# Optimization experiments

Hardware: AMD Instinct MI355X
Metric: run time of the kernel (lower is better)

## Reference

```python
import jax, jax.numpy as jnp
import numpy as np

B, S, D = 4, 2048, 1024
E = 16          # num_experts
K = 2           # num_experts_per_tok
F = 512         # moe_intermediate_size
FS = 2048       # shared_expert_intermediate_size


def setup_inputs() -> dict:
    key = jax.random.key(0)
    ks = jax.random.split(key, 9)
    s = 0.02
    return {
        "hidden_states": jax.random.normal(ks[0], (B, S, D), jnp.float32),
        "router_w": jax.random.normal(ks[1], (E, D), jnp.float32) * s,   # torch Linear-style [out,in]
        "Wg": jax.random.normal(ks[2], (E, D, F), jnp.float32) * s,      # gate_proj per expert
        "Wu": jax.random.normal(ks[3], (E, D, F), jnp.float32) * s,      # up_proj per expert
        "Wd": jax.random.normal(ks[4], (E, F, D), jnp.float32) * s,      # down_proj per expert
        "Sg": jax.random.normal(ks[5], (D, FS), jnp.float32) * s,        # shared expert gate_proj
        "Su": jax.random.normal(ks[6], (D, FS), jnp.float32) * s,        # shared expert up_proj
        "Sd": jax.random.normal(ks[7], (FS, D), jnp.float32) * s,        # shared expert down_proj
        "shared_gate_w": jax.random.normal(ks[8], (D, 1), jnp.float32) * s,
    }


def reference(hidden_states, router_w, Wg, Wu, Wd, Sg, Su, Sd, shared_gate_w):
    b, s, d = hidden_states.shape
    x = hidden_states.reshape(-1, d)                      # [T, D]
    T = x.shape[0]

    # --- router (Qwen3NextTopKRouter): fp32 softmax -> topk -> renorm ---
    logits = jnp.einsum("td,ed->te", x.astype(jnp.float32), router_w.astype(jnp.float32))
    probs = jax.nn.softmax(logits, axis=-1)               # [T, E]
    top_w, top_i = jax.lax.top_k(probs, K)                # [T, K]
    top_w = top_w / jnp.sum(top_w, axis=-1, keepdims=True)  # norm_topk_prob
    top_w = top_w.astype(x.dtype)

    # dense combine weights [T, E]: zero except at selected experts (index_add semantics)
    dense_w = jnp.zeros((T, E), x.dtype).at[jnp.arange(T)[:, None], top_i].add(top_w)

    # --- experts: SwiGLU per expert, scan over the fixed expert axis ---
    def body(acc, params):
        wg, wu, wd, cw = params                            # cw: [T]
        h = jax.nn.silu(x @ wg) * (x @ wu)                 # [T, F]
        return acc + cw[:, None] * (h @ wd), None

    expert_out, _ = jax.lax.scan(body, jnp.zeros_like(x), (Wg, Wu, Wd, dense_w.T))

    # --- shared expert with sigmoid gate ---
    shared = (jax.nn.silu(x @ Sg) * (x @ Su)) @ Sd         # [T, D]
    shared = jax.nn.sigmoid(x @ shared_gate_w) * shared

    out = expert_out + shared
    return out.reshape(b, s, d)
```

## Files before the change

kernel.cpp:

```cpp
#include <hip/hip_runtime.h>

typedef __attribute__((ext_vector_type(8))) short short8;
typedef __attribute__((ext_vector_type(4))) float f32x4;
typedef unsigned short u16;
typedef unsigned int u32;

#define DEVI __device__ __forceinline__

DEVI u16 f2b(float f) {
  u32 u = __float_as_uint(f);
  u32 r = u + 0x7FFFu + ((u >> 16) & 1u);
  return (u16)(r >> 16);
}
DEVI float b2f(u16 h) { return __uint_as_float(((u32)h) << 16); }
DEVI float silu(float g) { return g / (1.f + __expf(-g)); }

constexpr int T_ = 8192, D_ = 1024, E_ = 16, F_ = 512, FS_ = 2048;

constexpr size_t OFF_XB   = 0;
constexpr size_t OFF_WGU  = OFF_XB  + (size_t)T_ * D_ * 2;
constexpr size_t OFF_WDT  = OFF_WGU + (size_t)E_ * 2 * F_ * D_ * 2;
constexpr size_t OFF_SGU  = OFF_WDT + (size_t)E_ * D_ * F_ * 2;
constexpr size_t OFF_SDT  = OFF_SGU + (size_t)2 * FS_ * D_ * 2;
constexpr size_t OFF_HB   = OFF_SDT + (size_t)D_ * FS_ * 2;
constexpr size_t OFF_HS   = OFF_HB  + (size_t)2 * T_ * F_ * 2;
constexpr size_t OFF_PAIR = OFF_HS  + (size_t)T_ * FS_ * 2;
constexpr size_t OFF_PW   = OFF_PAIR + (size_t)2 * T_ * D_ * 2;
constexpr size_t OFF_GATE = OFF_PW  + (size_t)2 * T_ * 4;
constexpr size_t OFF_CNT  = OFF_GATE + (size_t)T_ * 4;
constexpr size_t OFF_TOP2 = OFF_CNT + 64;
constexpr size_t OFF_LIST = OFF_TOP2 + (size_t)T_ * 4;

__global__ void prep_kernel(
    const float4* __restrict__ x4, const float4* __restrict__ rw4,
    const float4* __restrict__ sgw4, int* __restrict__ top2e,
    float* __restrict__ pw, float* __restrict__ gate, ushort4* __restrict__ xb4,
    const float* __restrict__ Wg, const float* __restrict__ Wu, const float* __restrict__ Wd,
    const float* __restrict__ Sg, const float* __restrict__ Su, const float* __restrict__ Sd,
    u16* __restrict__ wgu, u16* __restrict__ wdT,
    u16* __restrict__ sgu, u16* __restrict__ sdT) {
  const int tid = threadIdx.x;
  const int bid = blockIdx.x;
  if (bid >= 7680) {
    const int lane = tid & 63, wid = tid >> 6;
    const int t = (bid - 7680) * 4 + wid;
    const float4* xr = x4 + (size_t)t * (D_ / 4);
    float acc[17];
#pragma unroll
    for (int e = 0; e < 17; ++e) acc[e] = 0.f;
    ushort4 xo[4];
#pragma unroll
    for (int j = 0; j < 4; ++j) {
      const int d4 = j * 64 + lane;
      float4 xv = xr[d4];
      xo[j] = make_ushort4(f2b(xv.x), f2b(xv.y), f2b(xv.z), f2b(xv.w));
#pragma unroll
      for (int e = 0; e < 16; ++e) {
        float4 wv = rw4[e * 256 + d4];
        acc[e] = fmaf(xv.x, wv.x, fmaf(xv.y, wv.y, fmaf(xv.z, wv.z, fmaf(xv.w, wv.w, acc[e]))));
      }
      float4 sv = sgw4[d4];
      acc[16] = fmaf(xv.x, sv.x, fmaf(xv.y, sv.y, fmaf(xv.z, sv.z, fmaf(xv.w, sv.w, acc[16]))));
    }
#pragma unroll
    for (int j = 0; j < 4; ++j)
      xb4[(size_t)t * 256 + j * 64 + lane] = xo[j];
#pragma unroll
    for (int e = 0; e < 17; ++e) {
      float v = acc[e];
#pragma unroll
      for (int off = 32; off; off >>= 1) v += __shfl_xor(v, off);
      acc[e] = v;
    }
    if (lane == 0) {
      int i1 = 0; float l1 = acc[0];
#pragma unroll
      for (int e = 1; e < 16; ++e) if (acc[e] > l1) { l1 = acc[e]; i1 = e; }
      int i2 = (i1 == 0) ? 1 : 0; float l2 = acc[i2];
#pragma unroll
      for (int e = 0; e < 16; ++e) {
        if (e == i1) continue;
        if (acc[e] > l2) { l2 = acc[e]; i2 = e; }
      }
      float w1 = 1.f / (1.f + expf(l2 - l1));
      top2e[t] = i1 | (i2 << 8);
      pw[2 * t] = w1;
      pw[2 * t + 1] = 1.f - w1;
      gate[t] = 1.f / (1.f + expf(-acc[16]));
    }
    return;
  }
  __shared__ float lds[64][65];
  int i = bid;
  const float* in; u16* out; int R, C, mode, rem;
  if (i < 6144) {
    int j = i >> 11; rem = i & 2047;
    int b = rem >> 7; rem &= 127;
    if (j == 0)      { in = Wg + (size_t)b * D_ * F_; out = wgu + (size_t)b * 2 * F_ * D_; R = D_; C = F_;  mode = 0; }
    else if (j == 1) { in = Wu + (size_t)b * D_ * F_; out = wgu + (size_t)b * 2 * F_ * D_; R = D_; C = F_;  mode = 1; }
    else             { in = Wd + (size_t)b * F_ * D_; out = wdT + (size_t)b * D_ * F_;     R = F_; C = D_;  mode = 2; }
  } else {
    int r2 = i - 6144; int j = r2 >> 9; rem = r2 & 511;
    if (j == 0)      { in = Sg; out = sgu; R = D_;  C = FS_; mode = 0; }
    else if (j == 1) { in = Su; out = sgu; R = D_;  C = FS_; mode = 1; }
    else             { in = Sd; out = sdT; R = FS_; C = D_;  mode = 2; }
  }
  const int ntx = C >> 6;
  const int cx = rem % ntx, cy = rem / ntx;
  const int c0 = cx * 64, r0 = cy * 64;
  {
    const int tx4 = (tid & 15) * 4, ty = tid >> 4;
#pragma unroll
    for (int p = 0; p < 4; ++p) {
      const int rr = ty + p * 16;
      float4 v = *(const float4*)&in[(size_t)(r0 + rr) * C + c0 + tx4];
      lds[rr][tx4] = v.x; lds[rr][tx4 + 1] = v.y; lds[rr][tx4 + 2] = v.z; lds[rr][tx4 + 3] = v.w;
    }
  }
  __syncthreads();
  {
    const int ol = tid >> 2, seg = tid & 3;
    const int f = c0 + ol;
    size_t orow;
    if (mode == 2) orow = f;
    else orow = (size_t)((f >> 4) << 5) + (f & 15) + (mode == 1 ? 16 : 0);
    u16 vals[16];
#pragma unroll
    for (int k = 0; k < 16; ++k) vals[k] = f2b(lds[seg * 16 + k][ol]);
    u16* dst = out + orow * R + r0 + seg * 16;
    *(short8*)dst = *(short8*)&vals[0];
    *(short8*)(dst + 8) = *(short8*)&vals[8];
  }
}

__global__ __launch_bounds__(1024) void compact_kernel(
    const int* __restrict__ top2e, int* __restrict__ lists, int* __restrict__ counts) {
  const int e = blockIdx.x;
  const int tid = threadIdx.x, lane = tid & 63, wid = tid >> 6;
  __shared__ int wsum[16];
  __shared__ int base;
  if (tid == 0) base = 0;
  __syncthreads();
  for (int c0 = 0; c0 < T_; c0 += 1024) {
    const int t = c0 + tid;
    const int pk = top2e[t];
    int slot = -1;
    if ((pk & 0xFF) == e) slot = 2 * t;
    else if (((pk >> 8) & 0xFF) == e) slot = 2 * t + 1;
    const unsigned long long m = __ballot(slot >= 0);
    const int myofs = __popcll(m & ((1ULL << lane) - 1ULL));
    if (lane == 0) wsum[wid] = __popcll(m);
    __syncthreads();
    const int b = base;
    int wbase = 0;
#pragma unroll
    for (int w = 0; w < 16; ++w) if (w < wid) wbase += wsum[w];
    if (slot >= 0) lists[e * T_ + b + wbase + myofs] = slot;
    __syncthreads();
    if (tid == 0) {
      int s = 0;
#pragma unroll
      for (int w = 0; w < 16; ++w) s += wsum[w];
      base += s;
    }
    __syncthreads();
  }
  if (tid == 0) counts[e] = base;
}

DEVI void gl_lds16(const void* gsrc, void* lds) {
  __builtin_amdgcn_global_load_lds((const __attribute__((address_space(1))) unsigned int*)gsrc,
                                   (__attribute__((address_space(3))) unsigned int*)lds, 16, 0, 0);
}

DEVI void prefix16(const int* counts, int e, int& cnt, int& roff) {
  cnt = counts[e];
  int s = 0;
#pragma unroll
  for (int k = 0; k < E_; ++k) s += (k < e) ? counts[k] : 0;
  roff = s;
}

__global__ __launch_bounds__(256, 4) void gu_gemm(
    const u16* __restrict__ xb, const u16* __restrict__ wgu, const u16* __restrict__ sgu,
    u16* __restrict__ hb, u16* __restrict__ hs,
    const int* __restrict__ counts, const int* __restrict__ lists) {
  extern __shared__ char smem[];
  const int tid = threadIdx.x;
  const int bid = blockIdx.x;
  const bool se = (bid >= 2048);
  int mt, nt, e = 0, cnt = 0, roff = 0;
  const u16* B0;
  if (!se) {
    e = bid >> 7; int r = bid & 127; mt = r >> 3; nt = r & 7;
    prefix16(counts, e, cnt, roff);
    if (mt * 128 >= cnt) return;
    B0 = wgu + (size_t)e * 2 * F_ * D_;
  } else {
    int st = bid - 2048;
    mt = st & 63; nt = st >> 6;
    B0 = sgu;
  }

  const int lane = tid & 63, wid = tid >> 6;
  const int wm = wid >> 1, wn = wid & 1;
  const int lr = lane & 15, lg = lane >> 4;
  const int ldsrow = tid >> 3;
  const int kslot = (tid & 7) << 4;
  constexpr size_t strideB = (size_t)D_ * 2;
  const char* aSrc[4]; const char* bSrc[4];
#pragma unroll
  for (int q = 0; q < 4; ++q) {
    int row = q * 32 + ldsrow;
    int kb = kslot ^ ((row & 7) << 4);
    int r = mt * 128 + row;
    long arow;
    if (!se) arow = (r < cnt) ? (lists[e * T_ + r] >> 1) : 0;
    else arow = r;
    aSrc[q] = (const char*)xb + (size_t)arow * strideB + kb;
    int nrow = nt * 128 + row;
    bSrc[q] = (const char*)B0 + (size_t)nrow * strideB + kb;
  }

  const f32x4 fz = {0.f, 0.f, 0.f, 0.f};
  f32x4 acc[4][4];
#pragma unroll
  for (int i = 0; i < 4; ++i)
#pragma unroll
    for (int j = 0; j < 4; ++j) acc[i][j] = fz;

  const int sw = (lr & 7) << 4;
  constexpr int nks = D_ / 64;

  for (int ks = 0; ks < nks; ++ks) {
    const int kbo = ks * 128;
#pragma unroll
    for (int q = 0; q < 4; ++q) gl_lds16(aSrc[q] + kbo, smem + q * 4096 + tid * 16);
#pragma unroll
    for (int q = 0; q < 4; ++q) gl_lds16(bSrc[q] + kbo, smem + 16384 + q * 4096 + tid * 16);
    __syncthreads();
    const char* As = smem;
    const char* Bs = smem + 16384;
#pragma unroll
    for (int kk = 0; kk < 2; ++kk) {
      const int ko = kk * 64 + lg * 16;
      short8 af[4];
#pragma unroll
      for (int fm = 0; fm < 4; ++fm) {
        int row = wm * 64 + fm * 16 + lr;
        af[fm] = *(const short8*)(As + row * 128 + (ko ^ sw));
      }
#pragma unroll
      for (int fn = 0; fn < 4; ++fn) {
        int col = wn * 64 + fn * 16 + lr;
        short8 bf = *(const short8*)(Bs + col * 128 + (ko ^ sw));
#pragma unroll
        for (int fm = 0; fm < 4; ++fm)
          acc[fm][fn] = __builtin_amdgcn_mfma_f32_16x16x32_bf16(af[fm], bf, acc[fm][fn], 0, 0, 0);
      }
    }
    __syncthreads();
  }

  const int c0 = 16 * (4 * nt + 2 * wn);
  const int r0 = mt * 128;
#pragma unroll
  for (int fm = 0; fm < 4; ++fm) {
#pragma unroll
    for (int j = 0; j < 4; ++j) {
      const int r = r0 + wm * 64 + fm * 16 + lg * 4 + j;
      if (!se && r >= cnt) continue;
      float h0 = silu(acc[fm][0][j]) * acc[fm][1][j];
      float h1 = silu(acc[fm][2][j]) * acc[fm][3][j];
      if (!se) {
        hb[(size_t)(roff + r) * F_ + c0 + lr] = f2b(h0);
        hb[(size_t)(roff + r) * F_ + c0 + 16 + lr] = f2b(h1);
      } else {
        hs[(size_t)r * FS_ + c0 + lr] = f2b(h0);
        hs[(size_t)r * FS_ + c0 + 16 + lr] = f2b(h1);
      }
    }
  }
}

template <int MODE>
__global__ __launch_bounds__(256, 4) void moe_gemm(
    const u16* __restrict__ Abase, const u16* __restrict__ B0,
    u16* __restrict__ outb, float* __restrict__ outf,
    const int* __restrict__ counts, const int* __restrict__ lists,
    const float* __restrict__ pw, const float* __restrict__ gate,
    const u16* __restrict__ pairb, int Kdim) {
  extern __shared__ char smem[];
  const int tid = threadIdx.x;
  const int mt = blockIdx.x, nt = blockIdx.y, e = blockIdx.z;

  int cnt = 0;
  const u16* A = Abase;
  if constexpr (MODE == 1) {
    int roff;
    prefix16(counts, e, cnt, roff);
    if (mt * 128 >= cnt) return;
    A = Abase + (size_t)roff * Kdim;
    B0 += (size_t)e * D_ * F_;
  }

  const int lane = tid & 63, wid = tid >> 6;
  const int wm = wid >> 1, wn = wid & 1;
  const int lr = lane & 15, lg = lane >> 4;
  const int ldsrow = tid >> 3;
  const int kslot = (tid & 7) << 4;
  const size_t strideB = (size_t)Kdim * 2;
  const char* aSrc[4]; const char* bSrc[4];
#pragma unroll
  for (int q = 0; q < 4; ++q) {
    int row = q * 32 + ldsrow;
    int kb = kslot ^ ((row & 7) << 4);
    long arow;
    if constexpr (MODE == 1) {
      int r = mt * 128 + row;
      arow = (r < cnt) ? r : (cnt - 1);
    } else {
      arow = mt * 128 + row;
    }
    aSrc[q] = (const char*)A + (size_t)arow * strideB + kb;
    int nrow = nt * 128 + row;
    bSrc[q] = (const char*)B0 + (size_t)nrow * strideB + kb;
  }

  const f32x4 fz = {0.f, 0.f, 0.f, 0.f};
  f32x4 acc[4][4];
#pragma unroll
  for (int i = 0; i < 4; ++i)
#pragma unroll
    for (int j = 0; j < 4; ++j) acc[i][j] = fz;

  const int nks = Kdim >> 6;
  const int sw = (lr & 7) << 4;

  for (int ks = 0; ks < nks; ++ks) {
    const int kbo = ks * 128;
#pragma unroll
    for (int q = 0; q < 4; ++q) gl_lds16(aSrc[q] + kbo, smem + q * 4096 + tid * 16);
#pragma unroll
    for (int q = 0; q < 4; ++q) gl_lds16(bSrc[q] + kbo, smem + 16384 + q * 4096 + tid * 16);
    __syncthreads();
    const char* As = smem;
    const char* Bs = smem + 16384;
#pragma unroll
    for (int kk = 0; kk < 2; ++kk) {
      const int ko = kk * 64 + lg * 16;
      short8 af[4];
#pragma unroll
      for (int fm = 0; fm < 4; ++fm) {
        int row = wm * 64 + fm * 16 + lr;
        af[fm] = *(const short8*)(As + row * 128 + (ko ^ sw));
      }
#pragma unroll
      for (int fn = 0; fn < 4; ++fn) {
        int col = wn * 64 + fn * 16 + lr;
        short8 bf = *(const short8*)(Bs + col * 128 + (ko ^ sw));
#pragma unroll
        for (int fm = 0; fm < 4; ++fm)
          acc[fm][fn] = __builtin_amdgcn_mfma_f32_16x16x32_bf16(af[fm], bf, acc[fm][fn], 0, 0, 0);
      }
    }
    __syncthreads();
  }

  const int r0 = mt * 128;
#pragma unroll
  for (int fm = 0; fm < 4; ++fm) {
#pragma unroll
    for (int j = 0; j < 4; ++j) {
      const int rowt = wm * 64 + fm * 16 + lg * 4 + j;
      const int r = r0 + rowt;
      if constexpr (MODE == 1) {
        if (r >= cnt) continue;
      }
      int slot = 0;
      float rsc = 0.f;
      if constexpr (MODE == 1) { slot = lists[e * T_ + r]; rsc = pw[slot]; }
      if constexpr (MODE == 3) rsc = gate[r];
#pragma unroll
      for (int fn = 0; fn < 4; ++fn) {
        const int c = nt * 128 + wn * 64 + fn * 16 + lr;
        float v = acc[fm][fn][j];
        if constexpr (MODE == 1) {
          outb[(size_t)slot * D_ + c] = f2b(rsc * v);
        } else {
          float o = v * rsc + b2f(pairb[(size_t)(2 * r) * D_ + c]) + b2f(pairb[(size_t)(2 * r + 1) * D_ + c]);
          outf[(size_t)r * D_ + c] = o;
        }
      }
    }
  }
}

extern "C" void kernel_launch(void* const* d_in, const int* in_sizes, int n_in,
                              void* d_out, int out_size, void* d_ws, size_t ws_size,
                              hipStream_t stream) {
  const float* x   = (const float*)d_in[0];
  const float* rw  = (const float*)d_in[1];
  const float* Wg  = (const float*)d_in[2];
  const float* Wu  = (const float*)d_in[3];
  const float* Wd  = (const float*)d_in[4];
  const float* Sg  = (const float*)d_in[5];
  const float* Su  = (const float*)d_in[6];
  const float* Sd  = (const float*)d_in[7];
  const float* sgw = (const float*)d_in[8];
  float* out = (float*)d_out;

  unsigned char* ws = (unsigned char*)d_ws;
  u16* xb    = (u16*)(ws + OFF_XB);
  u16* wgu   = (u16*)(ws + OFF_WGU);
  u16* wdT   = (u16*)(ws + OFF_WDT);
  u16* sgu   = (u16*)(ws + OFF_SGU);
  u16* sdT   = (u16*)(ws + OFF_SDT);
  u16* hb    = (u16*)(ws + OFF_HB);
  u16* hs    = (u16*)(ws + OFF_HS);
  u16* pairb = (u16*)(ws + OFF_PAIR);
  float* pwf   = (float*)(ws + OFF_PW);
  float* gatef = (float*)(ws + OFF_GATE);
  int* cnti    = (int*)(ws + OFF_CNT);
  int* top2i   = (int*)(ws + OFF_TOP2);
  int* listsi  = (int*)(ws + OFF_LIST);

  prep_kernel<<<9728, 256, 0, stream>>>(
      (const float4*)x, (const float4*)rw, (const float4*)sgw,
      top2i, pwf, gatef, (ushort4*)xb,
      Wg, Wu, Wd, Sg, Su, Sd, wgu, wdT, sgu, sdT);
  compact_kernel<<<E_, 1024, 0, stream>>>(top2i, listsi, cnti);

  gu_gemm<<<4096, 256, 32768, stream>>>(xb, wgu, sgu, hb, hs, cnti, listsi);
  moe_gemm<1><<<dim3(16, 8, 16), 256, 32768, stream>>>(hb, wdT, pairb, nullptr,
                                                       cnti, listsi, pwf, gatef, nullptr, 512);
  moe_gemm<3><<<dim3(64, 8, 1), 256, 32768, stream>>>(hs, sdT, nullptr, out,
                                                      cnti, listsi, pwf, gatef, pairb, 2048);

  (void)in_sizes; (void)n_in; (void)out_size; (void)ws_size;
}
```

Measured before the change: 273.3 us.

## Double-buffer LDS in shared-expert down GEMM and retune launch bounds

The shared-expert down-projection GEMM (MODE 3, K=2048) now uses two LDS stages of 32 KB each, so the next K-tile is fetched while MFMAs run on the current one, removing one barrier per iteration. Its dynamic LDS grows to 64 KB and its occupancy hint drops to 2 blocks per CU. Separately, gu_gemm and the routed moe_gemm raise their min-blocks-per-CU hint from 4 to 5, which may constrain register allocation and cause spills.

New measurement: 387.6 us. 41.8% more time.

```diff
diff --git a/kernel.cpp b/kernel.cpp
--- a/kernel.cpp
+++ b/kernel.cpp
@@ -181,7 +181,7 @@
   roff = s;
 }
 
-__global__ __launch_bounds__(256, 4) void gu_gemm(
+__global__ __launch_bounds__(256, 5) void gu_gemm(
     const u16* __restrict__ xb, const u16* __restrict__ wgu, const u16* __restrict__ sgu,
     u16* __restrict__ hb, u16* __restrict__ hs,
     const int* __restrict__ counts, const int* __restrict__ lists) {
@@ -284,7 +284,7 @@
 }
 
 template <int MODE>
-__global__ __launch_bounds__(256, 4) void moe_gemm(
+__global__ __launch_bounds__(256, MODE == 3 ? 2 : 5) void moe_gemm(
     const u16* __restrict__ Abase, const u16* __restrict__ B0,
     u16* __restrict__ outb, float* __restrict__ outf,
     const int* __restrict__ counts, const int* __restrict__ lists,
@@ -337,34 +337,78 @@
   const int nks = Kdim >> 6;
   const int sw = (lr & 7) << 4;
 
-  for (int ks = 0; ks < nks; ++ks) {
-    const int kbo = ks * 128;
-#pragma unroll
-    for (int q = 0; q < 4; ++q) gl_lds16(aSrc[q] + kbo, smem + q * 4096 + tid * 16);
-#pragma unroll
-    for (int q = 0; q < 4; ++q) gl_lds16(bSrc[q] + kbo, smem + 16384 + q * 4096 + tid * 16);
-    __syncthreads();
-    const char* As = smem;
-    const char* Bs = smem + 16384;
-#pragma unroll
-    for (int kk = 0; kk < 2; ++kk) {
-      const int ko = kk * 64 + lg * 16;
-      short8 af[4];
-#pragma unroll
-      for (int fm = 0; fm < 4; ++fm) {
-        int row = wm * 64 + fm * 16 + lr;
-        af[fm] = *(const short8*)(As + row * 128 + (ko ^ sw));
-      }
-#pragma unroll
-      for (int fn = 0; fn < 4; ++fn) {
-        int col = wn * 64 + fn * 16 + lr;
-        short8 bf = *(const short8*)(Bs + col * 128 + (ko ^ sw));
-#pragma unroll
-        for (int fm = 0; fm < 4; ++fm)
-          acc[fm][fn] = __builtin_amdgcn_mfma_f32_16x16x32_bf16(af[fm], bf, acc[fm][fn], 0, 0, 0);
-      }
-    }
-    __syncthreads();
+  if constexpr (MODE == 3) {
+    {
+      char* dst = smem;
+#pragma unroll
+      for (int q = 0; q < 4; ++q) gl_lds16(aSrc[q], dst + q * 4096 + tid * 16);
+#pragma unroll
+      for (int q = 0; q < 4; ++q) gl_lds16(bSrc[q], dst + 16384 + q * 4096 + tid * 16);
+    }
+    __syncthreads();
+    int cur = 0;
+    for (int ks = 0; ks < nks; ++ks) {
+      if (ks + 1 < nks) {
+        const int kbo = (ks + 1) * 128;
+        char* dst = smem + (cur ^ 1) * 32768;
+#pragma unroll
+        for (int q = 0; q < 4; ++q) gl_lds16(aSrc[q] + kbo, dst + q * 4096 + tid * 16);
+#pragma unroll
+        for (int q = 0; q < 4; ++q) gl_lds16(bSrc[q] + kbo, dst + 16384 + q * 4096 + tid * 16);
+      }
+      const char* As = smem + cur * 32768;
+      const char* Bs = As + 16384;
+#pragma unroll
+      for (int kk = 0; kk < 2; ++kk) {
+        const int ko = kk * 64 + lg * 16;
+        short8 af[4];
+#pragma unroll
+        for (int fm = 0; fm < 4; ++fm) {
+          int row = wm * 64 + fm * 16 + lr;
+          af[fm] = *(const short8*)(As + row * 128 + (ko ^ sw));
+        }
+#pragma unroll
+        for (int fn = 0; fn < 4; ++fn) {
+          int col = wn * 64 + fn * 16 + lr;
+          short8 bf = *(const short8*)(Bs + col * 128 + (ko ^ sw));
+#pragma unroll
+          for (int fm = 0; fm < 4; ++fm)
+            acc[fm][fn] = __builtin_amdgcn_mfma_f32_16x16x32_bf16(af[fm], bf, acc[fm][fn], 0, 0, 0);
+        }
+      }
+      __syncthreads();
+      cur ^= 1;
+    }
+  } else {
+    for (int ks = 0; ks < nks; ++ks) {
+      const int kbo = ks * 128;
+#pragma unroll
+      for (int q = 0; q < 4; ++q) gl_lds16(aSrc[q] + kbo, smem + q * 4096 + tid * 16);
+#pragma unroll
+      for (int q = 0; q < 4; ++q) gl_lds16(bSrc[q] + kbo, smem + 16384 + q * 4096 + tid * 16);
+      __syncthreads();
+      const char* As = smem;
+      const char* Bs = smem + 16384;
+#pragma unroll
+      for (int kk = 0; kk < 2; ++kk) {
+        const int ko = kk * 64 + lg * 16;
+        short8 af[4];
+#pragma unroll
+        for (int fm = 0; fm < 4; ++fm) {
+          int row = wm * 64 + fm * 16 + lr;
+          af[fm] = *(const short8*)(As + row * 128 + (ko ^ sw));
+        }
+#pragma unroll
+        for (int fn = 0; fn < 4; ++fn) {
+          int col = wn * 64 + fn * 16 + lr;
+          short8 bf = *(const short8*)(Bs + col * 128 + (ko ^ sw));
+#pragma unroll
+          for (int fm = 0; fm < 4; ++fm)
+            acc[fm][fn] = __builtin_amdgcn_mfma_f32_16x16x32_bf16(af[fm], bf, acc[fm][fn], 0, 0, 0);
+        }
+      }
+      __syncthreads();
+    }
   }
 
   const int r0 = mt * 128;
@@ -434,7 +478,7 @@
   gu_gemm<<<4096, 256, 32768, stream>>>(xb, wgu, sgu, hb, hs, cnti, listsi);
   moe_gemm<1><<<dim3(16, 8, 16), 256, 32768, stream>>>(hb, wdT, pairb, nullptr,
                                                        cnti, listsi, pwf, gatef, nullptr, 512);
-  moe_gemm<3><<<dim3(64, 8, 1), 256, 32768, stream>>>(hs, sdT, nullptr, out,
+  moe_gemm<3><<<dim3(64, 8, 1), 256, 65536, stream>>>(hs, sdT, nullptr, out,
                                                       cnti, listsi, pwf, gatef, pairb, 2048);
 
   (void)in_sizes; (void)n_in; (void)out_size; (void)ws_size;
```
